# Performance work log

Measured on AMD Instinct MI355X. Metric: run time of the kernel, lower is better.

The kernel has to match this reference:

```python
import jax, jax.numpy as jnp
import numpy as np

OUT_FEATURES = 4096
IN_FEATURES = 4096
SCALE_EPS = 1e-5


def setup_inputs() -> dict:
    key = jax.random.key(0)
    k1, k2, k3 = jax.random.split(key, 3)
    x = jax.random.normal(k1, (8192, IN_FEATURES), dtype=jnp.float32)
    # packed int4 weights: two signed nibbles per byte-equivalent int
    weight_packed = jax.random.randint(k2, (OUT_FEATURES, IN_FEATURES // 2), 0, 256, dtype=jnp.int32)
    weight_scale = jax.random.uniform(k3, (OUT_FEATURES,), dtype=jnp.float32) * 0.01 + 1e-4
    return {"x": x, "weight_packed": weight_packed, "weight_scale": weight_scale}


def _unpack_int4(weight_packed):
    # low nibble first, then high nibble, sign-extended from 4 bits
    low = weight_packed & 15
    high = (weight_packed >> 4) & 15
    low = jnp.where(low > 7, low - 16, low)
    high = jnp.where(high > 7, high - 16, high)
    # interleave -> [out_features, in_features]
    w_q = jnp.stack([low, high], axis=-1).reshape(weight_packed.shape[0], -1)
    return w_q


def reference(x, weight_packed, weight_scale):
    # per-row activation quantization to int4 range [-8, 7]
    x_max = jnp.max(jnp.abs(x), axis=-1, keepdims=True)
    x_scale = jnp.maximum(x_max / 7.0, SCALE_EPS)          # [tokens, 1]
    x_q = jnp.clip(jnp.round(x / x_scale), -8.0, 7.0)      # float carrier of int4 values

    w_q = _unpack_int4(weight_packed).astype(jnp.float32)  # [out, in]

    out = jnp.einsum('ti,oi->to', x_q, w_q)                # [tokens, out]
    out = out * (x_scale * weight_scale[None, :])
    return out.astype(x.dtype)
```

## Files before the change

### kernel.cpp

```cpp
#include <hip/hip_runtime.h>

#define SCALE_EPS 1e-5f

typedef int v4i __attribute__((ext_vector_type(4)));

static __device__ __forceinline__ void gll16(const void* g, void* l) {
  __builtin_amdgcn_global_load_lds(
      (const __attribute__((address_space(1))) unsigned int*)g,
      (__attribute__((address_space(3))) unsigned int*)l,
      16, 0, 0);
}


__global__ __launch_bounds__(256) void unpack_w(const int* __restrict__ wp,
                                                char* __restrict__ wq) {
  const int kc = blockIdx.x;
  const int nt = blockIdx.y;
  const int tid = threadIdx.x;
  char* tile = wq + ((size_t)nt * 64 + kc) * 4096;
  const int n0 = nt * 128;
#pragma unroll
  for (int gi = 0; gi < 2; ++gi) {
    int g = gi * 256 + tid;
    int r = g >> 2, cc = g & 3;
    const v4i* src = (const v4i*)(wp + (size_t)(n0 + r) * 2048 + kc * 32 + cc * 8);
    v4i m0 = src[0], m1 = src[1];
    unsigned int d0 =
        ((unsigned)m0.x & 15) | (((unsigned)m0.z & 15) << 4) |
        ((((unsigned)m0.x >> 4) & 15) << 8) | ((((unsigned)m0.z >> 4) & 15) << 12) |
        (((unsigned)m0.y & 15) << 16) | (((unsigned)m0.w & 15) << 20) |
        ((((unsigned)m0.y >> 4) & 15) << 24) | ((((unsigned)m0.w >> 4) & 15) << 28);
    unsigned int d1 =
        ((unsigned)m1.x & 15) | (((unsigned)m1.z & 15) << 4) |
        ((((unsigned)m1.x >> 4) & 15) << 8) | ((((unsigned)m1.z >> 4) & 15) << 12) |
        (((unsigned)m1.y & 15) << 16) | (((unsigned)m1.w & 15) << 20) |
        ((((unsigned)m1.y >> 4) & 15) << 24) | ((((unsigned)m1.w >> 4) & 15) << 28);
    d0 ^= 0x88888888u;
    d1 ^= 0x88888888u;
    *(uint2*)(tile + (r >> 5) * 1024 + cc * 256 + (r & 15) * 16 + ((r >> 4) & 1) * 8) =
        make_uint2(d0, d1);
  }
}

__global__ __launch_bounds__(256) void quant_x(const float* __restrict__ x,
                                               char* __restrict__ xq,
                                               float* __restrict__ xs,
                                               int* __restrict__ sa) {
  __shared__ float lmax[4][4];
  __shared__ int lsum[4][4];
  const int tid = threadIdx.x;
  const int w = tid >> 6;
  const int l = tid & 63;
  const int t0 = blockIdx.x * 4;
  const int row = l >> 4;
  const int t = t0 + row;
  const int sub = l & 15;

  const float* base = x + (size_t)t * 4096 + w * 1024 + sub * 4;
  float4 vals[16];
  float m = 0.0f;
#pragma unroll
  for (int s = 0; s < 16; ++s) {
    vals[s] = *(const float4*)(base + s * 64);
    m = fmaxf(m, fmaxf(fmaxf(fabsf(vals[s].x), fabsf(vals[s].y)),
                       fmaxf(fabsf(vals[s].z), fabsf(vals[s].w))));
  }
#pragma unroll
  for (int d = 1; d < 16; d <<= 1) m = fmaxf(m, __shfl_xor(m, d, 64));
  if (sub == 0) lmax[w][row] = m;
  __syncthreads();
  float rm = fmaxf(fmaxf(lmax[0][row], lmax[1][row]),
                   fmaxf(lmax[2][row], lmax[3][row]));
  float scale = fmaxf(rm / 7.0f, SCALE_EPS);
  if (w == 0 && sub == 0) xs[t] = scale;

  const int mt = t0 >> 7;
  const int f = (t0 & 127) >> 4;
  const int r16 = t & 15;
  const int cc = sub >> 2;
  const int b4 = (sub & 3) * 4;

  int isum = 0;
#pragma unroll
  for (int s = 0; s < 16; ++s) {
    float4 v = vals[s];
    int q0 = (int)fminf(fmaxf(rintf(v.x / scale), -8.0f), 7.0f);
    int q1 = (int)fminf(fmaxf(rintf(v.y / scale), -8.0f), 7.0f);
    int q2 = (int)fminf(fmaxf(rintf(v.z / scale), -8.0f), 7.0f);
    int q3 = (int)fminf(fmaxf(rintf(v.w / scale), -8.0f), 7.0f);
    isum += q0 + q1 + q2 + q3;
    unsigned int wd = (unsigned int)(q0 & 255) | ((unsigned int)(q1 & 255) << 8) |
                      ((unsigned int)(q2 & 255) << 16) | ((unsigned int)(q3 & 255) << 24);
    *(unsigned int*)(xq + ((size_t)mt * 64 + w * 16 + s) * 8192 +
                     f * 1024 + cc * 256 + r16 * 16 + b4) = wd;
  }
#pragma unroll
  for (int dd = 1; dd < 16; dd <<= 1) isum += __shfl_xor(isum, dd, 64);
  if (sub == 0) lsum[w][row] = isum;
  __syncthreads();
  if (w == 0 && sub == 0)
    sa[t] = lsum[0][row] + lsum[1][row] + lsum[2][row] + lsum[3][row];
}

__global__ __launch_bounds__(512, 2) void gemm_i8(const char* __restrict__ xq,
                                                  const char* __restrict__ wq,
                                                  const float* __restrict__ xs,
                                                  const int* __restrict__ sa,
                                                  const float* __restrict__ wsc,
                                                  float* __restrict__ out) {
  __shared__ char lds[4][24576];
  const int tid = threadIdx.x;
  const int wid = tid >> 6;
  const int lane = tid & 63;
  const int wm = wid >> 2;
  const int wn = wid & 3;

  const int bid = blockIdx.x;
  const int wg = (bid & 7) * 64 + (bid >> 3);
  const int by = wg >> 4;
  const int bx = wg & 15;

  const int toff = tid * 16;
  const char* aSrc0 = xq + (size_t)(2 * by) * 64 * 8192;
  const char* aSrc1 = aSrc0 + 64 * 8192;
  const char* bSrcT = wq + (size_t)(2 * bx + (toff >> 12)) * 262144 + (toff & 4095);
  const int aoff = (lane >> 4) * 256 + (lane & 15) * 16;
  const int laoff = lane * 16;

  v4i acc[8][4] = {};
  v4i fB[2][4];
  v4i aA0, aA1, aA2, aA3;
  v4i pB0, pB1;
  const unsigned MSK = 0x0f0f0f0fu;

#define LO4(w) (int)((unsigned)(w) & MSK)
#define HI4(w) (int)(((unsigned)(w) >> 4) & MSK)
#define UNPK(da, db, p)                                         \
  do {                                                          \
    da = (v4i){LO4((p).x), HI4((p).x), LO4((p).y), HI4((p).y)}; \
    db = (v4i){LO4((p).z), HI4((p).z), LO4((p).w), HI4((p).w)}; \
  } while (0)

#define STAGE3(kt)                                              \
  do {                                                          \
    char* d_ = lds[(kt) & 3];                                   \
    gll16(aSrc0 + (size_t)(kt) * 8192 + toff, d_ + toff);       \
    gll16(aSrc1 + (size_t)(kt) * 8192 + toff, d_ + 8192 + toff);\
    gll16(bSrcT + (size_t)(kt) * 4096, d_ + 16384 + toff);      \
  } while (0)

#define MF2(m0, m1, xx, yy, c)                                                         \
  do {                                                                                 \
    __builtin_amdgcn_s_setprio(1);                                                     \
    _Pragma("unroll") for (int ni = 0; ni < 4; ++ni) {                                 \
      acc[m0][ni] =                                                                    \
          __builtin_amdgcn_mfma_i32_16x16x64_i8(xx, fB[c][ni], acc[m0][ni], 0, 0, 0);  \
      acc[m1][ni] =                                                                    \
          __builtin_amdgcn_mfma_i32_16x16x64_i8(yy, fB[c][ni], acc[m1][ni], 0, 0, 0);  \
    }                                                                                  \
    __builtin_amdgcn_s_setprio(0);                                                     \
  } while (0)

#define TILE(c, kt, do_stage, do_next, vm)                                   \
  do {                                                                       \
    const char* Aw_ = lds[(kt) & 3] + wm * 8192 + laoff;                     \
    const char* Bn_ = lds[((kt) + 1) & 3] + 16384 + wn * 2048 + aoff;        \
    const char* An_ = lds[((kt) + 1) & 3] + wm * 8192 + laoff;               \
                                  \
    aA2 = *(const v4i*)(Aw_ + 2048);                                         \
    aA3 = *(const v4i*)(Aw_ + 3072);                                         \
    MF2(0, 1, aA0, aA1, c);                                                  \
                                  \
    aA0 = *(const v4i*)(Aw_ + 4096);                                         \
    aA1 = *(const v4i*)(Aw_ + 5120);                                         \
    MF2(2, 3, aA2, aA3, c);                                                  \
                            \
    if ((vm) == 3) asm volatile("s_waitcnt vmcnt(3)" ::: "memory");          \
    else if ((vm) == 0) asm volatile("s_waitcnt vmcnt(0)" ::: "memory");     \
    __builtin_amdgcn_s_barrier();                                            \
    __builtin_amdgcn_sched_barrier(0);                                       \
        \
    if (do_stage) STAGE3((kt) + 3);                                          \
    aA2 = *(const v4i*)(Aw_ + 6144);                                         \
    aA3 = *(const v4i*)(Aw_ + 7168);                                         \
    if (do_next) pB0 = *(const v4i*)(Bn_);                                   \
    MF2(4, 5, aA0, aA1, c);                                                  \
     \
    if (do_next) {                                                           \
      pB1 = *(const v4i*)(Bn_ + 1024);                                       \
      aA0 = *(const v4i*)(An_);                                              \
      aA1 = *(const v4i*)(An_ + 1024);                                       \
    }                                                                        \
    MF2(6, 7, aA2, aA3, c);                                                  \
    if (do_next) {                                                           \
      UNPK(fB[1 - (c)][0], fB[1 - (c)][1], pB0);                             \
      UNPK(fB[1 - (c)][2], fB[1 - (c)][3], pB1);                             \
    }                                                                        \
  } while (0)

  STAGE3(0); STAGE3(1); STAGE3(2);
  asm volatile("s_waitcnt vmcnt(6)" ::: "memory");
  __builtin_amdgcn_s_barrier();
  __builtin_amdgcn_sched_barrier(0);
  {
    const char* B0_ = lds[0] + 16384 + wn * 2048 + aoff;
    pB0 = *(const v4i*)(B0_);
    pB1 = *(const v4i*)(B0_ + 1024);
    aA0 = *(const v4i*)(lds[0] + wm * 8192 + laoff);
    aA1 = *(const v4i*)(lds[0] + wm * 8192 + laoff + 1024);
    UNPK(fB[0][0], fB[0][1], pB0);
    UNPK(fB[0][2], fB[0][3], pB1);
  }

  for (int kt = 0; kt < 60; kt += 2) {
    TILE(0, kt, 1, 1, 3);
    TILE(1, kt + 1, 1, 1, 3);
  }
  TILE(0, 60, 1, 1, 3);
  TILE(1, 61, 0, 1, 3);
  TILE(0, 62, 0, 1, 0);
  TILE(1, 63, 0, 0, -1);

#undef TILE
#undef MF2
#undef STAGE3
#undef UNPK
#undef LO4
#undef HI4

  float wvv[4];
#pragma unroll
  for (int ni = 0; ni < 4; ++ni)
    wvv[ni] = wsc[bx * 256 + wn * 64 + ni * 16 + (lane & 15)];
  const int rbase = by * 256 + wm * 128 + ((lane >> 4) << 2);
  const int cbase = bx * 256 + wn * 64 + (lane & 15);
#pragma unroll
  for (int mi = 0; mi < 8; ++mi) {
#pragma unroll
    for (int j = 0; j < 4; ++j) {
      int t = rbase + mi * 16 + j;
      int sat = sa[t];
      float xsv = xs[t];
      float* orow = out + (size_t)t * 4096 + cbase;
#pragma unroll
      for (int ni = 0; ni < 4; ++ni) {
        int cv = acc[mi][ni][j] - 8 * sat;
        orow[ni * 16] = (float)cv * (xsv * wvv[ni]);
      }
    }
  }
}

extern "C" void kernel_launch(void* const* d_in, const int* in_sizes, int n_in,
                              void* d_out, int out_size, void* d_ws, size_t ws_size,
                              hipStream_t stream) {
  const float* x = (const float*)d_in[0];
  const int* wp = (const int*)d_in[1];
  const float* wsc = (const float*)d_in[2];
  float* out = (float*)d_out;
  char* ws = (char*)d_ws;

  char* xq = ws;
  char* wq = ws + 33554432;
  float* xs = (float*)(ws + 41943040);
  int* sa = (int*)(ws + 41943040 + 32768);

  hipLaunchKernelGGL(unpack_w, dim3(64, 32), dim3(256), 0, stream, wp, wq);
  hipLaunchKernelGGL(quant_x, dim3(2048), dim3(256), 0, stream, x, xq, xs, sa);
  hipLaunchKernelGGL(gemm_i8, dim3(512), dim3(512), 0, stream, xq, wq, xs, sa, wsc, out);
}
```

Baseline: 168.2 us.

## Switch int8 GEMM to 32x32x32 MFMA with matching operand layouts

Replaces the 16x16x64 int8 MFMA tiling with 32x32x32 int8 MFMA instructions, changing the accumulator shape to 16-wide vectors. The packed layouts written by the weight-unpack and activation-quant kernels are rearranged so each lane can load its 32x32 operand fragment with a single 16-byte LDS read, and the epilogue is rewritten for the new output mapping. The aim is to cut MFMA instruction count and the LDS reads per unit of math. The larger instructions can lengthen dependency chains and change register pressure.

Measured after the change: 175.6 us. 4.4% more time.

```diff
diff --git a/kernel.cpp b/kernel.cpp
--- a/kernel.cpp
+++ b/kernel.cpp
@@ -3,6 +3,7 @@
 #define SCALE_EPS 1e-5f
 
 typedef int v4i __attribute__((ext_vector_type(4)));
+typedef int v16i __attribute__((ext_vector_type(16)));
 
 static __device__ __forceinline__ void gll16(const void* g, void* l) {
   __builtin_amdgcn_global_load_lds(
@@ -37,7 +38,8 @@
         ((((unsigned)m1.y >> 4) & 15) << 24) | ((((unsigned)m1.w >> 4) & 15) << 28);
     d0 ^= 0x88888888u;
     d1 ^= 0x88888888u;
-    *(uint2*)(tile + (r >> 5) * 1024 + cc * 256 + (r & 15) * 16 + ((r >> 4) & 1) * 8) =
+    *(uint2*)(tile + (r >> 6) * 2048 + (cc >> 1) * 1024 +
+              ((cc & 1) * 32 + (r & 31)) * 16 + ((r >> 5) & 1) * 8) =
         make_uint2(d0, d1);
   }
 }
@@ -74,11 +76,10 @@
   float scale = fmaxf(rm / 7.0f, SCALE_EPS);
   if (w == 0 && sub == 0) xs[t] = scale;
 
-  const int mt = t0 >> 7;
-  const int f = (t0 & 127) >> 4;
-  const int r16 = t & 15;
-  const int cc = sub >> 2;
-  const int b4 = (sub & 3) * 4;
+  const int mt = t >> 7;
+  const int rb = (t & 127) >> 5;
+  char* dst0 = xq + (size_t)mt * 64 * 8192 + rb * 2048 + (sub >> 3) * 1024 +
+               ((sub >> 2) & 1) * 512 + (t & 31) * 16 + (sub & 3) * 4;
 
   int isum = 0;
 #pragma unroll
@@ -91,8 +92,7 @@
     isum += q0 + q1 + q2 + q3;
     unsigned int wd = (unsigned int)(q0 & 255) | ((unsigned int)(q1 & 255) << 8) |
                       ((unsigned int)(q2 & 255) << 16) | ((unsigned int)(q3 & 255) << 24);
-    *(unsigned int*)(xq + ((size_t)mt * 64 + w * 16 + s) * 8192 +
-                     f * 1024 + cc * 256 + r16 * 16 + b4) = wd;
+    *(unsigned int*)(dst0 + (size_t)(w * 16 + s) * 8192) = wd;
   }
 #pragma unroll
   for (int dd = 1; dd < 16; dd <<= 1) isum += __shfl_xor(isum, dd, 64);
@@ -124,12 +124,11 @@
   const char* aSrc0 = xq + (size_t)(2 * by) * 64 * 8192;
   const char* aSrc1 = aSrc0 + 64 * 8192;
   const char* bSrcT = wq + (size_t)(2 * bx + (toff >> 12)) * 262144 + (toff & 4095);
-  const int aoff = (lane >> 4) * 256 + (lane & 15) * 16;
   const int laoff = lane * 16;
 
-  v4i acc[8][4] = {};
+  v16i acc[4][2] = {};
   v4i fB[2][4];
-  v4i aA0, aA1, aA2, aA3;
+  v4i aa0, aa1, aa2, aa3;
   v4i pB0, pB1;
   const unsigned MSK = 0x0f0f0f0fu;
 
@@ -149,49 +148,52 @@
     gll16(bSrcT + (size_t)(kt) * 4096, d_ + 16384 + toff);      \
   } while (0)
 
-#define MF2(m0, m1, xx, yy, c)                                                         \
-  do {                                                                                 \
-    __builtin_amdgcn_s_setprio(1);                                                     \
-    _Pragma("unroll") for (int ni = 0; ni < 4; ++ni) {                                 \
-      acc[m0][ni] =                                                                    \
-          __builtin_amdgcn_mfma_i32_16x16x64_i8(xx, fB[c][ni], acc[m0][ni], 0, 0, 0);  \
-      acc[m1][ni] =                                                                    \
-          __builtin_amdgcn_mfma_i32_16x16x64_i8(yy, fB[c][ni], acc[m1][ni], 0, 0, 0);  \
-    }                                                                                  \
-    __builtin_amdgcn_s_setprio(0);                                                     \
+#define MFQ(rb0_, xx, yy, c, ks)                                               \
+  do {                                                                         \
+    __builtin_amdgcn_s_setprio(1);                                             \
+    acc[rb0_][0] = __builtin_amdgcn_mfma_i32_32x32x32_i8(                      \
+        xx, fB[c][(ks) * 2], acc[rb0_][0], 0, 0, 0);                           \
+    acc[rb0_][1] = __builtin_amdgcn_mfma_i32_32x32x32_i8(                      \
+        xx, fB[c][(ks) * 2 + 1], acc[rb0_][1], 0, 0, 0);                       \
+    acc[rb0_ + 1][0] = __builtin_amdgcn_mfma_i32_32x32x32_i8(                  \
+        yy, fB[c][(ks) * 2], acc[rb0_ + 1][0], 0, 0, 0);                       \
+    acc[rb0_ + 1][1] = __builtin_amdgcn_mfma_i32_32x32x32_i8(                  \
+        yy, fB[c][(ks) * 2 + 1], acc[rb0_ + 1][1], 0, 0, 0);                   \
+    __builtin_amdgcn_s_setprio(0);                                             \
   } while (0)
 
 #define TILE(c, kt, do_stage, do_next, vm)                                   \
   do {                                                                       \
     const char* Aw_ = lds[(kt) & 3] + wm * 8192 + laoff;                     \
-    const char* Bn_ = lds[((kt) + 1) & 3] + 16384 + wn * 2048 + aoff;        \
+    const char* Bn_ = lds[((kt) + 1) & 3] + 16384 + (wn >> 1) * 4096 +       \
+                      (wn & 1) * 2048 + laoff;                               \
     const char* An_ = lds[((kt) + 1) & 3] + wm * 8192 + laoff;               \
-                                  \
-    aA2 = *(const v4i*)(Aw_ + 2048);                                         \
-    aA3 = *(const v4i*)(Aw_ + 3072);                                         \
-    MF2(0, 1, aA0, aA1, c);                                                  \
-                                  \
-    aA0 = *(const v4i*)(Aw_ + 4096);                                         \
-    aA1 = *(const v4i*)(Aw_ + 5120);                                         \
-    MF2(2, 3, aA2, aA3, c);                                                  \
+                       \
+    aa2 = *(const v4i*)(Aw_ + 4096);                                         \
+    aa3 = *(const v4i*)(Aw_ + 6144);                                         \
+    MFQ(0, aa0, aa1, c, 0);                                                  \
+                       \
+    aa0 = *(const v4i*)(Aw_ + 1024);                                         \
+    aa1 = *(const v4i*)(Aw_ + 3072);                                         \
+    MFQ(2, aa2, aa3, c, 0);                                                  \
                             \
     if ((vm) == 3) asm volatile("s_waitcnt vmcnt(3)" ::: "memory");          \
     else if ((vm) == 0) asm volatile("s_waitcnt vmcnt(0)" ::: "memory");     \
     __builtin_amdgcn_s_barrier();                                            \
     __builtin_amdgcn_sched_barrier(0);                                       \
-        \
+     \
     if (do_stage) STAGE3((kt) + 3);                                          \
-    aA2 = *(const v4i*)(Aw_ + 6144);                                         \
-    aA3 = *(const v4i*)(Aw_ + 7168);                                         \
+    aa2 = *(const v4i*)(Aw_ + 5120);                                         \
+    aa3 = *(const v4i*)(Aw_ + 7168);                                         \
     if (do_next) pB0 = *(const v4i*)(Bn_);                                   \
-    MF2(4, 5, aA0, aA1, c);                                                  \
-     \
+    MFQ(0, aa0, aa1, c, 1);                                                  \
+           \
     if (do_next) {                                                           \
       pB1 = *(const v4i*)(Bn_ + 1024);                                       \
-      aA0 = *(const v4i*)(An_);                                              \
-      aA1 = *(const v4i*)(An_ + 1024);                                       \
+      aa0 = *(const v4i*)(An_);                                              \
+      aa1 = *(const v4i*)(An_ + 2048);                                       \
     }                                                                        \
-    MF2(6, 7, aA2, aA3, c);                                                  \
+    MFQ(2, aa2, aa3, c, 1);                                                  \
     if (do_next) {                                                           \
       UNPK(fB[1 - (c)][0], fB[1 - (c)][1], pB0);                             \
       UNPK(fB[1 - (c)][2], fB[1 - (c)][3], pB1);                             \
@@ -203,11 +205,12 @@
   __builtin_amdgcn_s_barrier();
   __builtin_amdgcn_sched_barrier(0);
   {
-    const char* B0_ = lds[0] + 16384 + wn * 2048 + aoff;
+    const char* A0_ = lds[0] + wm * 8192 + laoff;
+    const char* B0_ = lds[0] + 16384 + (wn >> 1) * 4096 + (wn & 1) * 2048 + laoff;
+    aa0 = *(const v4i*)(A0_);
+    aa1 = *(const v4i*)(A0_ + 2048);
     pB0 = *(const v4i*)(B0_);
     pB1 = *(const v4i*)(B0_ + 1024);
-    aA0 = *(const v4i*)(lds[0] + wm * 8192 + laoff);
-    aA1 = *(const v4i*)(lds[0] + wm * 8192 + laoff + 1024);
     UNPK(fB[0][0], fB[0][1], pB0);
     UNPK(fB[0][2], fB[0][3], pB1);
   }
@@ -222,30 +225,29 @@
   TILE(1, 63, 0, 0, -1);
 
 #undef TILE
-#undef MF2
+#undef MFQ
 #undef STAGE3
 #undef UNPK
 #undef LO4
 #undef HI4
 
-  float wvv[4];
-#pragma unroll
-  for (int ni = 0; ni < 4; ++ni)
-    wvv[ni] = wsc[bx * 256 + wn * 64 + ni * 16 + (lane & 15)];
-  const int rbase = by * 256 + wm * 128 + ((lane >> 4) << 2);
-  const int cbase = bx * 256 + wn * 64 + (lane & 15);
-#pragma unroll
-  for (int mi = 0; mi < 8; ++mi) {
-#pragma unroll
-    for (int j = 0; j < 4; ++j) {
-      int t = rbase + mi * 16 + j;
-      int sat = sa[t];
-      float xsv = xs[t];
-      float* orow = out + (size_t)t * 4096 + cbase;
-#pragma unroll
-      for (int ni = 0; ni < 4; ++ni) {
-        int cv = acc[mi][ni][j] - 8 * sat;
-        orow[ni * 16] = (float)cv * (xsv * wvv[ni]);
+  float wv0 = wsc[bx * 256 + wn * 64 + (lane & 31)];
+  float wv1 = wsc[bx * 256 + wn * 64 + 32 + (lane & 31)];
+  const int cb = bx * 256 + wn * 64 + (lane & 31);
+  const int rw = by * 256 + wm * 128 + ((lane >> 5) << 2);
+#pragma unroll
+  for (int rb = 0; rb < 4; ++rb) {
+#pragma unroll
+    for (int g = 0; g < 4; ++g) {
+#pragma unroll
+      for (int j = 0; j < 4; ++j) {
+        int row = rw + rb * 32 + g * 8 + j;
+        int reg = g * 4 + j;
+        int sv = sa[row];
+        float s = xs[row];
+        float* orow = out + (size_t)row * 4096 + cb;
+        orow[0]  = (float)(acc[rb][0][reg] - 8 * sv) * (s * wv0);
+        orow[32] = (float)(acc[rb][1][reg] - 8 * sv) * (s * wv1);
       }
     }
   }
```
